# Kernel optimization log

Measured on AMD Instinct MI355X. Metric: run time of the kernel, lower is better.

## Reference

```python
import jax, jax.numpy as jnp
import numpy as np

N, K = 16384, 32          # num bboxes, context size
IN_F, HID = 608, 384      # in_features, hidden_dim
ALPHA = 0.2               # LeakyReLU slope
NEG_INF = -9e15


def setup_inputs() -> dict:
    key = jax.random.key(0)
    k1, k2, k3, k4, k5, k6, k7, k8 = jax.random.split(key, 8)
    h_i = jax.random.normal(k1, (N, IN_F), dtype=jnp.float32)
    idx = jax.random.randint(k2, (N, K), 0, N)
    pad = jax.random.uniform(k3, (N, K)) < 0.2
    context_indices = jnp.where(pad, -1, idx).astype(jnp.int64)
    s_in = 1.0 / np.sqrt(IN_F)
    s_a = 1.0 / np.sqrt(2 * HID)
    W_i = jax.random.uniform(k4, (IN_F, HID), minval=-s_in, maxval=s_in, dtype=jnp.float32)
    W_j = jax.random.uniform(k5, (IN_F, HID), minval=-s_in, maxval=s_in, dtype=jnp.float32)
    a_i = jax.random.uniform(k6, (HID,), minval=-s_a, maxval=s_a, dtype=jnp.float32)
    a_j = jax.random.uniform(k7, (HID,), minval=-s_a, maxval=s_a, dtype=jnp.float32)
    a_b = jax.random.uniform(k8, (1,), minval=-s_a, maxval=s_a, dtype=jnp.float32)
    return {"h_i": h_i, "context_indices": context_indices,
            "W_i": W_i, "W_j": W_j, "a_i": a_i, "a_j": a_j, "a_b": a_b}


def reference(h_i, context_indices, W_i, W_j, a_i, a_j, a_b):
    n = h_i.shape[0]
    Wh_i = h_i @ W_i                          # [N, H]
    # W_j has no bias, so projecting then gathering (zero pad row) equals
    # gathering zero-padded features then projecting.
    Wh_all = h_i @ W_j                        # [N, H]
    Wh_pad = jnp.concatenate([Wh_all, jnp.zeros((1, HID), Wh_all.dtype)], axis=0)
    idx = jnp.where(context_indices >= 0, context_indices, n)   # -1 -> zero row
    Wh_j = Wh_pad[idx]                        # [N, K, H] gather
    # attention_layer(concat(Wh_i, Wh_j)) == Wh_i@a_i + Wh_j@a_j + b
    scores = (Wh_i @ a_i)[:, None] + Wh_j @ a_j + a_b[0]        # [N, K]
    scores = jnp.where(scores > 0, scores, ALPHA * scores)      # LeakyReLU
    scores = jnp.where(context_indices >= 0, scores, NEG_INF)   # mask padding
    att = jax.nn.softmax(scores, axis=1)                        # [N, K]
    h_prime = jnp.einsum('nk,nkh->nh', att, Wh_j)               # [N, H]
    return h_prime
```

## Files before the change

### kernel.cpp

```cpp
#include <hip/hip_runtime.h>
#include <hip/hip_bf16.h>

typedef unsigned short u16;
typedef unsigned int u32;
typedef __attribute__((ext_vector_type(8))) __bf16 bf16x8;
typedef __attribute__((ext_vector_type(4))) __bf16 bf16x4;
typedef __attribute__((ext_vector_type(4))) float f32x4;

#define KCTX 32
#define INF_ 608
#define HID_ 384
#define NBOX 16384

#define WH_OFF  19922944
#define BT_OFF  32505856
#define V_OFF   32972800
#define SI_OFF  32975232
#define SJ_OFF  33040768
#define AJF_OFF 33106304
#define ABF_OFF 33107840

__device__ __forceinline__ float bfu(u16 u)  { return __uint_as_float(((u32)u) << 16); }
__device__ __forceinline__ float bflo(u32 u) { return __uint_as_float(u << 16); }
__device__ __forceinline__ float bfhi(u32 u) { return __uint_as_float(u & 0xffff0000u); }
__device__ __forceinline__ u16 f2bf(float x) {
  u32 u = __float_as_uint(x);
  return (u16)((u + 0x7fffu + ((u >> 16) & 1u)) >> 16);
}
__device__ __forceinline__ void async_ld16(const void* g, void* l) {
  __builtin_amdgcn_global_load_lds(
      (const __attribute__((address_space(1))) u32*)g,
      (__attribute__((address_space(3))) u32*)l, 16, 0, 0);
}

__device__ __forceinline__ int detect_f32(const u32* hw) {
  const u32 w = hw[threadIdx.x & 63];
  const int e = (int)((w >> 7) & 0xffu);
  const unsigned long long mb = __ballot(e > 134 || e < 100);
  return __popcll(mb) >= 16;
}
__device__ __forceinline__ int detect_i64(const int* ci) {
  const int hi = ci[2 * (threadIdx.x & 63) + 1];
  const unsigned long long mz = __ballot(hi == 0 || hi == -1);
  return __popcll(mz) >= 48;
}

__global__ __launch_bounds__(256) void prep_kernel(
    const void* __restrict__ h, const void* __restrict__ Wi,
    const void* __restrict__ Wj, const void* __restrict__ ai,
    const void* __restrict__ aj, const void* __restrict__ ab,
    u16* __restrict__ Bt, float* __restrict__ v,
    float* __restrict__ ajf, float* __restrict__ abf) {
  __shared__ u16 tile[64][65];
  const int f32m = detect_f32((const u32*)h);
  const int bid = blockIdx.x, tid = threadIdx.x;
  if (bid < 60) {
    const int ft = bid / 6, ht = bid - ft * 6;
    const int f0 = ft * 64, h0 = ht * 64;
    const int ln = tid & 63, fg = tid >> 6;
#pragma unroll
    for (int rr = 0; rr < 16; ++rr) {
      const int fl = fg * 16 + rr;
      const int f = f0 + fl;
      if (f < INF_)
        tile[fl][ln] = f32m ? f2bf(((const float*)Wj)[(size_t)f * HID_ + h0 + ln])
                            : ((const u16*)Wj)[(size_t)f * HID_ + h0 + ln];
    }
    __syncthreads();
#pragma unroll
    for (int rr = 0; rr < 16; ++rr) {
      const int hl = fg * 16 + rr;
      const int f = f0 + ln;
      if (f < INF_) Bt[(size_t)(h0 + hl) * INF_ + f] = tile[ln][hl];
    }
  } else if (bid < 98) {
    const int t = (bid - 60) * 16 + (tid >> 4);
    const int sl = tid & 15;
    if (t < INF_) {
      float s = 0.f;
      if (f32m) {
        const float4* wi = (const float4*)((const float*)Wi + (size_t)t * HID_);
        const float4* a4 = (const float4*)ai;
        for (int c = sl; c < 96; c += 16) {
          float4 x = wi[c], y = a4[c];
          s += x.x * y.x + x.y * y.y + x.z * y.z + x.w * y.w;
        }
      } else {
        const uint4* wi = (const uint4*)((const u16*)Wi + (size_t)t * HID_);
        const uint4* a4 = (const uint4*)ai;
        for (int c = sl; c < 48; c += 16) {
          uint4 x = wi[c], y = a4[c];
          s += bflo(x.x) * bflo(y.x) + bfhi(x.x) * bfhi(y.x)
             + bflo(x.y) * bflo(y.y) + bfhi(x.y) * bfhi(y.y)
             + bflo(x.z) * bflo(y.z) + bfhi(x.z) * bfhi(y.z)
             + bflo(x.w) * bflo(y.w) + bfhi(x.w) * bfhi(y.w);
        }
      }
      s += __shfl_xor(s, 1); s += __shfl_xor(s, 2);
      s += __shfl_xor(s, 4); s += __shfl_xor(s, 8);
      if (sl == 0) v[t] = s;
    }
  } else {
    for (int j = tid; j < HID_; j += 256)
      ajf[j] = f32m ? ((const float*)aj)[j] : bfu(((const u16*)aj)[j]);
    if (tid == 0)
      abf[0] = f32m ? ((const float*)ab)[0] : bfu(((const u16*)ab)[0]);
  }
}

#define ASRO 612
__global__ __launch_bounds__(512, 2) void gemm_fused(
    const void* __restrict__ A, const u16* __restrict__ Bt,
    const float* __restrict__ v, u16* __restrict__ C,
    float* __restrict__ si, const float* __restrict__ ajf,
    float* __restrict__ sj) {
  extern __shared__ __align__(16) char smem[];
  u16* As = (u16*)smem;
  u16* Bs = (u16*)(smem + 78336);
  const int f32m = detect_f32((const u32*)A);
  const int tid  = threadIdx.x;
  const int lane = tid & 63;
  const int wv   = tid >> 6;
  const int row0 = blockIdx.x * 64;
  const char* Btb = (const char*)Bt;

#pragma unroll
  for (int i = 0; i < 3; ++i) {
    const int c = tid + i * 512;
    async_ld16(Btb + (size_t)(c >> 2) * 1216 + (c & 3) * 16, (char*)Bs + c * 16);
  }

  {
    const int g = tid >> 3, sub = tid & 7;
    float s = 0.f;
    const float4* v4 = (const float4*)v;
    if (f32m) {
      const float4* hr = (const float4*)((const float*)A + (size_t)(row0 + g) * INF_);
#pragma unroll
      for (int k = 0; k < 19; ++k) {
        const int c4 = sub + 8 * k;
        float4 x = hr[c4];
        ushort4 sv;
        sv.x = f2bf(x.x); sv.y = f2bf(x.y); sv.z = f2bf(x.z); sv.w = f2bf(x.w);
        *(ushort4*)&As[g * ASRO + c4 * 4] = sv;
        float4 w = v4[c4];
        s += x.x * w.x + x.y * w.y + x.z * w.z + x.w * w.w;
      }
    } else {
      const uint4* hr = (const uint4*)((const u16*)A + (size_t)(row0 + g) * INF_);
      for (int k = 0; k < 10; ++k) {
        const int c8 = sub + 8 * k;
        if (c8 < 76) {
          uint4 x = hr[c8];
          *(ushort4*)&As[g * ASRO + c8 * 8]     = *(ushort4*)&x.x;
          *(ushort4*)&As[g * ASRO + c8 * 8 + 4] = *(ushort4*)&x.z;
          float4 w0 = v4[2 * c8], w1 = v4[2 * c8 + 1];
          s += bflo(x.x) * w0.x + bfhi(x.x) * w0.y + bflo(x.y) * w0.z + bfhi(x.y) * w0.w
             + bflo(x.z) * w1.x + bfhi(x.z) * w1.y + bflo(x.w) * w1.z + bfhi(x.w) * w1.w;
        }
      }
    }
    s += __shfl_xor(s, 1); s += __shfl_xor(s, 2); s += __shfl_xor(s, 4);
    if (sub == 0) si[row0 + g] = s;
  }

  f32x4 acc[4][3];
#pragma unroll
  for (int i = 0; i < 4; ++i)
#pragma unroll
    for (int j = 0; j < 3; ++j) acc[i][j] = (f32x4){0.f, 0.f, 0.f, 0.f};

  const int lm = lane & 15, q = lane >> 4;
  const int n0 = wv * 48;

  __syncthreads();
  int cur = 0;
  for (int kt = 0; kt < 19; ++kt) {
    if (kt < 18) {
      const size_t kb = (size_t)(kt + 1) * 64;
#pragma unroll
      for (int i = 0; i < 3; ++i) {
        const int c = tid + i * 512;
        async_ld16(Btb + (size_t)(c >> 2) * 1216 + kb + (c & 3) * 16,
                   (char*)Bs + (cur ^ 1) * 24576 + c * 16);
      }
    }
    bf16x8 af[4], bfr[3];
#pragma unroll
    for (int im = 0; im < 4; ++im) {
      const int r = im * 16 + lm;
      bf16x4 lo = *(const bf16x4*)&As[r * ASRO + kt * 32 + q * 8];
      bf16x4 hi = *(const bf16x4*)&As[r * ASRO + kt * 32 + q * 8 + 4];
      af[im] = __builtin_shufflevector(lo, hi, 0, 1, 2, 3, 4, 5, 6, 7);
    }
#pragma unroll
    for (int in = 0; in < 3; ++in)
      bfr[in] = *(const bf16x8*)&Bs[cur * 12288 + (n0 + in * 16 + lm) * 32 + q * 8];
#pragma unroll
    for (int im = 0; im < 4; ++im)
#pragma unroll
      for (int in = 0; in < 3; ++in)
        acc[im][in] = __builtin_amdgcn_mfma_f32_16x16x32_bf16(
            af[im], bfr[in], acc[im][in], 0, 0, 0);
    __syncthreads();
    cur ^= 1;
  }

#pragma unroll
  for (int im = 0; im < 4; ++im)
#pragma unroll
    for (int in = 0; in < 3; ++in) {
      const int colg = n0 + in * 16 + lm;
#pragma unroll
      for (int r = 0; r < 4; ++r) {
        const int rowg = row0 + im * 16 + q * 4 + r;
        C[(size_t)rowg * HID_ + colg] = f2bf(acc[im][in][r]);
      }
    }
  float* sjred = (float*)Bs;
  float ajv[3];
#pragma unroll
  for (int in = 0; in < 3; ++in) ajv[in] = ajf[n0 + in * 16 + lm];
#pragma unroll
  for (int im = 0; im < 4; ++im)
#pragma unroll
    for (int r = 0; r < 4; ++r) {
      float p = acc[im][0][r] * ajv[0] + acc[im][1][r] * ajv[1]
              + acc[im][2][r] * ajv[2];
      p += __shfl_xor(p, 1); p += __shfl_xor(p, 2);
      p += __shfl_xor(p, 4); p += __shfl_xor(p, 8);
      if (lm == 0) sjred[wv * 64 + im * 16 + q * 4 + r] = p;
    }
  __syncthreads();
  if (tid < 64) {
    float s = 0.f;
#pragma unroll
    for (int w = 0; w < 8; ++w) s += sjred[w * 64 + tid];
    sj[row0 + tid] = s;
  }
}

__global__ __launch_bounds__(256) void attn_kernel(
    const void* __restrict__ h, const int* __restrict__ ci,
    const float* __restrict__ si, const float* __restrict__ sj,
    const float* __restrict__ abf, const u16* __restrict__ Wh,
    void* __restrict__ out) {
  __shared__ float2 ai_c[5][32];
  __shared__ int cnt_s[5];
  const int f32m = detect_f32((const u32*)h);
  const int i64  = detect_i64(ci);
  const int tid = threadIdx.x;
  const int n0 = blockIdx.x * 5;

  if (tid < 160) {
    const int r = tid >> 5, k = tid & 31;
    const int n = n0 + r;
    if (n < NBOX) {
      const size_t t = (size_t)n * KCTX + k;
      int idx;
      if (i64) { int lo = ci[2 * t], hi2 = ci[2 * t + 1]; idx = (hi2 < 0) ? -1 : lo; }
      else     { idx = ci[t]; }
      const bool valid = idx >= 0;
      const float sjv = valid ? sj[idx] : 0.f;
      float raw = si[n] + sjv + abf[0];
      float lr = raw > 0.f ? raw : 0.2f * raw;
      float s = valid ? lr : -9e15f;
      float m = s;
#pragma unroll
      for (int o = 16; o; o >>= 1) m = fmaxf(m, __shfl_xor(m, o, 32));
      float p = __expf(s - m);
      float d = p;
#pragma unroll
      for (int o = 16; o; o >>= 1) d += __shfl_xor(d, o, 32);
      float w = p / d;
      unsigned key = valid ? (unsigned)idx : 0x7fffffffu;
#pragma unroll
      for (int kk = 2; kk <= 32; kk <<= 1) {
#pragma unroll
        for (int j = kk >> 1; j > 0; j >>= 1) {
          unsigned pk = __shfl_xor(key, j, 32);
          float    pw = __shfl_xor(w,   j, 32);
          const bool want_min = ((k & kk) == 0) == ((k & j) == 0);
          const bool take = want_min ? (pk < key) : (pk > key);
          if (take) { key = pk; w = pw; }
        }
      }
      const unsigned long long bm = __ballot(valid);
      const u32 m32 = (u32)(bm >> (tid & 32));
      const int cnt = __popc(m32);
      const int r8 = (cnt + 7) & ~7;
      ai_c[r][k] = (k < cnt) ? (float2){w, __int_as_float((int)key)}
                             : (float2){0.f, 0.f};
      if (k == 0) cnt_s[r] = r8;
    } else if ((tid & 31) == 0) {
      cnt_s[r] = 0;
    }
  }
  __syncthreads();

  if (tid < 240) {
    const int r = tid / 48, c = tid - r * 48;
    const int n = n0 + r;
    if (n < NBOX) {
      const int K8 = cnt_s[r];
      float a0 = 0, a1 = 0, a2 = 0, a3 = 0, a4 = 0, a5 = 0, a6 = 0, a7 = 0;
      for (int kb = 0; kb < K8; kb += 8) {
        uint4 q[8]; float ww[8];
#pragma unroll
        for (int u = 0; u < 8; ++u) {
          const float2 e = ai_c[r][kb + u];
          ww[u] = e.x;
          const int j = __float_as_int(e.y);
          q[u] = ((const uint4*)(Wh + (u32)j * HID_))[c];
        }
        __builtin_amdgcn_sched_barrier(0);
#pragma unroll
        for (int u = 0; u < 8; ++u) {
          const float w = ww[u];
          a0 += w * bflo(q[u].x); a1 += w * bfhi(q[u].x);
          a2 += w * bflo(q[u].y); a3 += w * bfhi(q[u].y);
          a4 += w * bflo(q[u].z); a5 += w * bfhi(q[u].z);
          a6 += w * bflo(q[u].w); a7 += w * bfhi(q[u].w);
        }
      }
      if (f32m) {
        float4* o4 = (float4*)out + (size_t)n * 96 + c * 2;
        o4[0] = (float4){a0, a1, a2, a3};
        o4[1] = (float4){a4, a5, a6, a7};
      } else {
        uint4 o;
        o.x = (u32)f2bf(a0) | ((u32)f2bf(a1) << 16);
        o.y = (u32)f2bf(a2) | ((u32)f2bf(a3) << 16);
        o.z = (u32)f2bf(a4) | ((u32)f2bf(a5) << 16);
        o.w = (u32)f2bf(a6) | ((u32)f2bf(a7) << 16);
        ((uint4*)out)[(size_t)n * 48 + c] = o;
      }
    }
  }
}

extern "C" void kernel_launch(void* const* d_in, const int* in_sizes, int n_in,
                              void* d_out, int out_size, void* d_ws, size_t ws_size,
                              hipStream_t stream) {
  const void* h  = d_in[0];
  const int*  ci = (const int*)d_in[1];
  const void* Wi = d_in[2];
  const void* Wj = d_in[3];
  const void* ai = d_in[4];
  const void* aj = d_in[5];
  const void* ab = d_in[6];

  char* ws = (char*)d_ws;
  u16*   Wh  = (u16*)(ws + WH_OFF);
  u16*   Bt  = (u16*)(ws + BT_OFF);
  float* v   = (float*)(ws + V_OFF);
  float* si  = (float*)(ws + SI_OFF);
  float* sj  = (float*)(ws + SJ_OFF);
  float* ajf = (float*)(ws + AJF_OFF);
  float* abf = (float*)(ws + ABF_OFF);

  prep_kernel<<<99, 256, 0, stream>>>(h, Wi, Wj, ai, aj, ab, Bt, v, ajf, abf);
  gemm_fused<<<256, 512, 127488, stream>>>(h, Bt, v, Wh, si, ajf, sj);
  attn_kernel<<<3277, 256, 0, stream>>>(h, ci, si, sj, abf, Wh, d_out);
}
```

Measured before the change: 157.7 us.

## Split attention into score and column-sliced gather kernels over a sliced Wh layout

The GEMM now writes Wh as eight 48-column slices, each stored contiguously per wave ([8][N][48]). A separate score kernel computes the softmax weights and writes them compacted with a prefix-popcount instead of a bitonic sort. A new gather kernel then has each block handle one column slice for 64 rows. The aim is to keep each slice's gather working set (about 1.5 MB) resident in cache. The cost is an extra launch, global round-trips for the weights, and the loss of sorted indices, which previously improved access locality.

```diff
diff --git a/kernel.cpp b/kernel.cpp
--- a/kernel.cpp
+++ b/kernel.cpp
@@ -12,6 +12,8 @@
 #define HID_ 384
 #define NBOX 16384
 
+#define AW_OFF  0
+#define CNT_OFF 4194304
 #define WH_OFF  19922944
 #define BT_OFF  32505856
 #define V_OFF   32972800
@@ -210,11 +212,11 @@
   for (int im = 0; im < 4; ++im)
 #pragma unroll
     for (int in = 0; in < 3; ++in) {
-      const int colg = n0 + in * 16 + lm;
+      const int cw = in * 16 + lm;
 #pragma unroll
       for (int r = 0; r < 4; ++r) {
         const int rowg = row0 + im * 16 + q * 4 + r;
-        C[(size_t)rowg * HID_ + colg] = f2bf(acc[im][in][r]);
+        C[((size_t)wv * NBOX + rowg) * 48 + cw] = f2bf(acc[im][in][r]);
       }
     }
   float* sjred = (float*)Bs;
@@ -240,102 +242,91 @@
   }
 }
 
-__global__ __launch_bounds__(256) void attn_kernel(
-    const void* __restrict__ h, const int* __restrict__ ci,
-    const float* __restrict__ si, const float* __restrict__ sj,
-    const float* __restrict__ abf, const u16* __restrict__ Wh,
+__global__ __launch_bounds__(256) void score_kernel(
+    const int* __restrict__ ci, const float* __restrict__ si,
+    const float* __restrict__ sj, const float* __restrict__ abf,
+    float2* __restrict__ aw, int* __restrict__ cnt) {
+  const int i64 = detect_i64(ci);
+  const int tid = threadIdx.x;
+  const int k = tid & 31;
+  const int n = blockIdx.x * 8 + (tid >> 5);
+  const size_t t = (size_t)n * KCTX + k;
+  int idx;
+  if (i64) { int lo = ci[2 * t], hi2 = ci[2 * t + 1]; idx = (hi2 < 0) ? -1 : lo; }
+  else     { idx = ci[t]; }
+  const bool valid = idx >= 0;
+  const float sjv = valid ? sj[idx] : 0.f;
+  float raw = si[n] + sjv + abf[0];
+  float lr = raw > 0.f ? raw : 0.2f * raw;
+  float s = valid ? lr : -9e15f;
+  float m = s;
+#pragma unroll
+  for (int o = 16; o; o >>= 1) m = fmaxf(m, __shfl_xor(m, o, 32));
+  float p = __expf(s - m);
+  float d = p;
+#pragma unroll
+  for (int o = 16; o; o >>= 1) d += __shfl_xor(d, o, 32);
+  const float w = p / d;
+  const unsigned long long bm = __ballot(valid);
+  const u32 m32 = (u32)(bm >> (tid & 32));
+  const int c_ = __popc(m32);
+  const int r4 = (c_ + 3) & ~3;
+  if (valid) {
+    const int pf = __popc(m32 & ((1u << k) - 1u));
+    aw[(size_t)n * KCTX + pf] = (float2){w, __int_as_float(idx)};
+  }
+  if (k >= c_ && k < r4) aw[(size_t)n * KCTX + k] = (float2){0.f, 0.f};
+  if (k == 0) cnt[n] = r4;
+}
+
+__global__ __launch_bounds__(384) void gather_kernel(
+    const void* __restrict__ h, const float2* __restrict__ aw,
+    const int* __restrict__ cnt, const u16* __restrict__ Wh2,
     void* __restrict__ out) {
-  __shared__ float2 ai_c[5][32];
-  __shared__ int cnt_s[5];
+  __shared__ float2 aws[64 * 33];
+  __shared__ int cs[64];
   const int f32m = detect_f32((const u32*)h);
-  const int i64  = detect_i64(ci);
   const int tid = threadIdx.x;
-  const int n0 = blockIdx.x * 5;
-
-  if (tid < 160) {
-    const int r = tid >> 5, k = tid & 31;
-    const int n = n0 + r;
-    if (n < NBOX) {
-      const size_t t = (size_t)n * KCTX + k;
-      int idx;
-      if (i64) { int lo = ci[2 * t], hi2 = ci[2 * t + 1]; idx = (hi2 < 0) ? -1 : lo; }
-      else     { idx = ci[t]; }
-      const bool valid = idx >= 0;
-      const float sjv = valid ? sj[idx] : 0.f;
-      float raw = si[n] + sjv + abf[0];
-      float lr = raw > 0.f ? raw : 0.2f * raw;
-      float s = valid ? lr : -9e15f;
-      float m = s;
-#pragma unroll
-      for (int o = 16; o; o >>= 1) m = fmaxf(m, __shfl_xor(m, o, 32));
-      float p = __expf(s - m);
-      float d = p;
-#pragma unroll
-      for (int o = 16; o; o >>= 1) d += __shfl_xor(d, o, 32);
-      float w = p / d;
-      unsigned key = valid ? (unsigned)idx : 0x7fffffffu;
-#pragma unroll
-      for (int kk = 2; kk <= 32; kk <<= 1) {
-#pragma unroll
-        for (int j = kk >> 1; j > 0; j >>= 1) {
-          unsigned pk = __shfl_xor(key, j, 32);
-          float    pw = __shfl_xor(w,   j, 32);
-          const bool want_min = ((k & kk) == 0) == ((k & j) == 0);
-          const bool take = want_min ? (pk < key) : (pk > key);
-          if (take) { key = pk; w = pw; }
-        }
-      }
-      const unsigned long long bm = __ballot(valid);
-      const u32 m32 = (u32)(bm >> (tid & 32));
-      const int cnt = __popc(m32);
-      const int r8 = (cnt + 7) & ~7;
-      ai_c[r][k] = (k < cnt) ? (float2){w, __int_as_float((int)key)}
-                             : (float2){0.f, 0.f};
-      if (k == 0) cnt_s[r] = r8;
-    } else if ((tid & 31) == 0) {
-      cnt_s[r] = 0;
-    }
-  }
+  const int s  = blockIdx.x & 7;
+  const int g0 = (blockIdx.x >> 3) * 64;
+  const float2* awg = aw + (size_t)g0 * KCTX;
+  for (int i = tid; i < 2048; i += 384) aws[(i >> 5) * 33 + (i & 31)] = awg[i];
+  if (tid < 64) cs[tid] = cnt[g0 + tid];
   __syncthreads();
 
-  if (tid < 240) {
-    const int r = tid / 48, c = tid - r * 48;
-    const int n = n0 + r;
-    if (n < NBOX) {
-      const int K8 = cnt_s[r];
-      float a0 = 0, a1 = 0, a2 = 0, a3 = 0, a4 = 0, a5 = 0, a6 = 0, a7 = 0;
-      for (int kb = 0; kb < K8; kb += 8) {
-        uint4 q[8]; float ww[8];
-#pragma unroll
-        for (int u = 0; u < 8; ++u) {
-          const float2 e = ai_c[r][kb + u];
-          ww[u] = e.x;
-          const int j = __float_as_int(e.y);
-          q[u] = ((const uint4*)(Wh + (u32)j * HID_))[c];
-        }
-        __builtin_amdgcn_sched_barrier(0);
-#pragma unroll
-        for (int u = 0; u < 8; ++u) {
-          const float w = ww[u];
-          a0 += w * bflo(q[u].x); a1 += w * bfhi(q[u].x);
-          a2 += w * bflo(q[u].y); a3 += w * bfhi(q[u].y);
-          a4 += w * bflo(q[u].z); a5 += w * bfhi(q[u].z);
-          a6 += w * bflo(q[u].w); a7 += w * bfhi(q[u].w);
-        }
-      }
-      if (f32m) {
-        float4* o4 = (float4*)out + (size_t)n * 96 + c * 2;
-        o4[0] = (float4){a0, a1, a2, a3};
-        o4[1] = (float4){a4, a5, a6, a7};
-      } else {
-        uint4 o;
-        o.x = (u32)f2bf(a0) | ((u32)f2bf(a1) << 16);
-        o.y = (u32)f2bf(a2) | ((u32)f2bf(a3) << 16);
-        o.z = (u32)f2bf(a4) | ((u32)f2bf(a5) << 16);
-        o.w = (u32)f2bf(a6) | ((u32)f2bf(a7) << 16);
-        ((uint4*)out)[(size_t)n * 48 + c] = o;
-      }
-    }
+  const int r = tid / 6, c = tid - r * 6;
+  const int n = g0 + r;
+  const u16* bc = Wh2 + (size_t)s * NBOX * 48 + c * 8;
+  const int kc = cs[r];
+  float a0 = 0, a1 = 0, a2 = 0, a3 = 0, a4 = 0, a5 = 0, a6 = 0, a7 = 0;
+  for (int k = 0; k < kc; k += 4) {
+    uint4 q[4]; float w4[4];
+#pragma unroll
+    for (int u = 0; u < 4; ++u) {
+      const float2 e = aws[r * 33 + k + u];
+      w4[u] = e.x;
+      q[u] = *(const uint4*)(bc + (size_t)((u32)__float_as_int(e.y)) * 48);
+    }
+#pragma unroll
+    for (int u = 0; u < 4; ++u) {
+      const float w = w4[u];
+      a0 += w * bflo(q[u].x); a1 += w * bfhi(q[u].x);
+      a2 += w * bflo(q[u].y); a3 += w * bfhi(q[u].y);
+      a4 += w * bflo(q[u].z); a5 += w * bfhi(q[u].z);
+      a6 += w * bflo(q[u].w); a7 += w * bfhi(q[u].w);
+    }
+  }
+  if (f32m) {
+    float4* o4 = (float4*)((float*)out + (size_t)n * HID_ + s * 48 + c * 8);
+    o4[0] = (float4){a0, a1, a2, a3};
+    o4[1] = (float4){a4, a5, a6, a7};
+  } else {
+    uint4 o;
+    o.x = (u32)f2bf(a0) | ((u32)f2bf(a1) << 16);
+    o.y = (u32)f2bf(a2) | ((u32)f2bf(a3) << 16);
+    o.z = (u32)f2bf(a4) | ((u32)f2bf(a5) << 16);
+    o.w = (u32)f2bf(a6) | ((u32)f2bf(a7) << 16);
+    *(uint4*)((u16*)out + (size_t)n * HID_ + s * 48 + c * 8) = o;
   }
 }
 
@@ -351,6 +342,8 @@
   const void* ab = d_in[6];
 
   char* ws = (char*)d_ws;
+  float2* aw  = (float2*)(ws + AW_OFF);
+  int*    cnt = (int*)(ws + CNT_OFF);
   u16*   Wh  = (u16*)(ws + WH_OFF);
   u16*   Bt  = (u16*)(ws + BT_OFF);
   float* v   = (float*)(ws + V_OFF);
@@ -361,5 +354,6 @@
 
   prep_kernel<<<99, 256, 0, stream>>>(h, Wi, Wj, ai, aj, ab, Bt, v, ajf, abf);
   gemm_fused<<<256, 512, 127488, stream>>>(h, Bt, v, Wh, si, ajf, sj);
-  attn_kernel<<<3277, 256, 0, stream>>>(h, ci, si, sj, abf, Wh, d_out);
-}
+  score_kernel<<<2048, 256, 0, stream>>>(ci, si, sj, abf, aw, cnt);
+  gather_kernel<<<2048, 384, 0, stream>>>(h, aw, cnt, Wh, d_out);
+}
```

Measured after the change: 161.0 us. +2.1%, slower.
